# Optimization experiments

Measured on AMD Instinct MI355X. Metric: run time of the kernel, lower is better.

## Reference

```python
import jax, jax.numpy as jnp
import numpy as np

B, S = 8, 1024                      # num sequences, per-seq prefill length (uniform ragged batch)
NUM_HEADS, HEAD_DIM, NUM_KV_HEADS = 32, 128, 8
GROUP = NUM_HEADS // NUM_KV_HEADS   # GQA repeat factor
SCALE = 1.0 / float(np.sqrt(HEAD_DIM))
T = B * S                           # total tokens in batch
NUM_SLOTS = 16384                   # KV-cache slots
DKV = NUM_KV_HEADS * HEAD_DIM


def setup_inputs() -> dict:
    key = jax.random.key(0)
    ks = jax.random.split(key, 4)
    q = jax.random.normal(ks[0], (T, NUM_HEADS * HEAD_DIM), dtype=jnp.float32)
    k = jax.random.normal(ks[1], (T, DKV), dtype=jnp.float32)
    v = jax.random.normal(ks[2], (T, DKV), dtype=jnp.float32)
    k_cache = jnp.zeros((NUM_SLOTS, DKV), dtype=jnp.float32)
    v_cache = jnp.zeros((NUM_SLOTS, DKV), dtype=jnp.float32)
    # distinct slots per token (pure prefill: gather mapping == store mapping)
    slot_mapping = jax.random.permutation(ks[3], NUM_SLOTS)[:T].astype(jnp.int32)
    seq_slot_mapping = slot_mapping
    return {"q": q, "k": k, "v": v, "k_cache": k_cache, "v_cache": v_cache,
            "slot_mapping": slot_mapping, "seq_slot_mapping": seq_slot_mapping}


def reference(q, k, v, k_cache, v_cache, slot_mapping, seq_slot_mapping):
    # reshape to per-head layout
    kr = k.reshape(T, DKV)
    vr = v.reshape(T, DKV)
    # store_kvcache: scatter new k/v into paged cache by slot
    k_cache = k_cache.at[slot_mapping].set(kr)
    v_cache = v_cache.at[slot_mapping].set(vr)
    # get_kvcache: gather the per-sequence contiguous KV from the cache
    ck = k_cache[seq_slot_mapping].reshape(B, S, NUM_KV_HEADS, HEAD_DIM)
    cv = v_cache[seq_slot_mapping].reshape(B, S, NUM_KV_HEADS, HEAD_DIM)
    qb = q.reshape(B, S, NUM_HEADS, HEAD_DIM)
    # GQA: repeat_interleave kv heads (matches torch SDPA enable_gqa)
    ck = jnp.repeat(ck, GROUP, axis=2)  # [B,S,H,D]
    cv = jnp.repeat(cv, GROUP, axis=2)
    scores = jnp.einsum("bqhd,bkhd->bhqk", qb, ck) * SCALE  # [B,H,S,S]
    causal = jnp.tril(jnp.ones((S, S), dtype=bool))
    scores = jnp.where(causal[None, None], scores, jnp.finfo(scores.dtype).min)
    probs = jax.nn.softmax(scores, axis=-1)
    o = jnp.einsum("bhqk,bkhd->bqhd", probs, cv)  # [B,S,H,D]
    return o.reshape(T, NUM_HEADS * HEAD_DIM)
```

## Files before the change

kernel.cpp:

```cpp
#include <hip/hip_runtime.h>

#define NB 8
#define NS 1024
#define NH 32
#define NKV 8
#define ND 128
#define QT 256
#define KT 64

typedef _Float16 f16x8 __attribute__((ext_vector_type(8)));
typedef __fp16 fp16x2 __attribute__((ext_vector_type(2)));
typedef float f32x16 __attribute__((ext_vector_type(16)));
typedef unsigned int u32x2 __attribute__((ext_vector_type(2)));

__device__ __forceinline__ float exp2fast(float x) { return __builtin_amdgcn_exp2f(x); }
__device__ __forceinline__ unsigned pkrtz_u(float a, float b) {
  union { fp16x2 h; unsigned u; } c;
  c.h = __builtin_amdgcn_cvt_pkrtz(a, b);
  return c.u;
}
__device__ __forceinline__ u32x2 swap32(float x) {
  union { float f; unsigned u; } c; c.f = x;
  return __builtin_amdgcn_permlane32_swap(c.u, c.u, false, false);
}
__device__ __forceinline__ float asf(unsigned u) { union { unsigned u; float f; } c; c.u = u; return c.f; }

__global__ __launch_bounds__(256)
void cvt_kf(const float* __restrict__ kg, char* __restrict__ wsK)
{
  int g = blockIdx.x * 256 + threadIdx.x;
  int t = g >> 7, c8 = g & 127;
  int hkv = c8 >> 4, d8 = c8 & 15;
  const float* src = kg + (size_t)t * 1024 + hkv * 128 + d8 * 8;
  float4 a = *(const float4*)src;
  float4 c = *(const float4*)(src + 4);
  f16x8 h8;
  h8[0] = (_Float16)a.x; h8[1] = (_Float16)a.y; h8[2] = (_Float16)a.z; h8[3] = (_Float16)a.w;
  h8[4] = (_Float16)c.x; h8[5] = (_Float16)c.y; h8[6] = (_Float16)c.z; h8[7] = (_Float16)c.w;
  int b  = t >> 10, kv = t & 1023;
  int ti = kv >> 6, kvl = kv & 63, kb = kvl >> 5, lq = kvl & 31;
  int dblk = d8 >> 1, hi = d8 & 1;
  size_t off = (((size_t)(b * 8 + hkv) * 16 + ti) * 16 + kb * 8 + dblk) * 1024 + (hi * 32 + lq) * 16;
  *(f16x8*)(wsK + off) = h8;
}

__global__ __launch_bounds__(256)
void cvt_vf(const float* __restrict__ vg, _Float16* __restrict__ wsV)
{
  __shared__ _Float16 T[ND][KT];
  const int tid = threadIdx.x;
  const int kvt = blockIdx.x, b = blockIdx.y, hkv = blockIdx.z;
#pragma unroll
  for (int pass = 0; pass < 8; ++pass) {
    int kvr = (tid >> 5) + pass * 8;
    int d4  = (tid & 31) * 4;
    float4 v = ((const float4*)vg)[(size_t)(b * NS + kvt * KT + kvr) * 256 + hkv * 32 + (tid & 31)];
    T[d4 + 0][kvr] = (_Float16)v.x;
    T[d4 + 1][kvr] = (_Float16)v.y;
    T[d4 + 2][kvr] = (_Float16)v.z;
    T[d4 + 3][kvr] = (_Float16)v.w;
  }
  __syncthreads();
  _Float16* out = wsV + ((size_t)(b * 8 + hkv) * 16 + kvt) * 8192;
#pragma unroll
  for (int pass = 0; pass < 4; ++pass) {
    int unit = tid + pass * 256;
    int c = unit >> 6, lane = unit & 63;
    int d = (c & 3) * 32 + (lane & 31);
    int kv8 = (c >> 2) * 16 + (lane >> 5) * 8;
    *(f16x8*)(out + unit * 8) = *(const f16x8*)&T[d][kv8];
  }
}

__global__ __launch_bounds__(512, 1)
void attn_fwd(const float* __restrict__ qg, const char* __restrict__ wsK,
              const char* __restrict__ wsV, float* __restrict__ og)
{
  __shared__ __align__(16) char Klds[4][16384];
  __shared__ __align__(16) char Vlds[4][16384];

  const int id = blockIdx.x;
  const int v  = (id & 7) * 32 + (id >> 3);
  const int panel = v >> 2;
  const int sub   = v & 3;
  const int b     = panel >> 3;
  const int hkv   = panel & 7;
  const int h     = hkv * 4 + sub;

  const int tid  = threadIdx.x;
  const int lane = tid & 63;
  const int w    = tid >> 6;
  const int lq   = lane & 31;
  const int hi   = lane >> 5;

  const float QS = 0.08838834764831845f * 1.4426950408889634f;

  const char* wsKb = wsK + (size_t)panel * 16 * 16384;
  const char* wsVb = wsV + (size_t)panel * 16 * 16384;

  const int o0 = tid * 16;
  const int o1 = (tid + 512) * 16;

  f16x8 kpre0, kpre1, vpre0, vpre1;

  const int qorder[4] = {0, 3, 1, 2};

#pragma unroll 1
  for (int ph = 0; ph < 4; ++ph) {
    const int qtile = qorder[ph];
    const int wv    = (ph & 1) ? (7 - w) : w;
    const int qr0w  = qtile * QT + wv * 32;
    const int qrow  = qr0w + lq;

    f16x8 qf[8];
    {
      const float* qp = qg + (size_t)(b * NS + qrow) * (NH * ND) + h * ND + hi * 8;
#pragma unroll
      for (int dblk = 0; dblk < 8; ++dblk) {
        float4 f0 = *(const float4*)(qp + dblk * 16);
        float4 f1 = *(const float4*)(qp + dblk * 16 + 4);
        f16x8 a;
        a[0] = (_Float16)(f0.x * QS); a[1] = (_Float16)(f0.y * QS);
        a[2] = (_Float16)(f0.z * QS); a[3] = (_Float16)(f0.w * QS);
        a[4] = (_Float16)(f1.x * QS); a[5] = (_Float16)(f1.y * QS);
        a[6] = (_Float16)(f1.z * QS); a[7] = (_Float16)(f1.w * QS);
        qf[dblk] = a;
      }
    }

    f32x16 acc[4];
#pragma unroll
    for (int nb = 0; nb < 4; ++nb)
#pragma unroll
      for (int r = 0; r < 16; ++r) acc[nb][r] = 0.f;
    float m_run = -1e30f, l_run = 0.f;

    auto compute_tile = [&](int t) {
      const int kv0 = t * KT;
      if (kv0 > qr0w + 31) return;
      const char* Kb = &Klds[t & 3][0];
      const char* Vb = &Vlds[t & 3][0];

      f32x16 s[2];
#pragma unroll
      for (int r = 0; r < 16; ++r) { s[0][r] = 0.f; s[1][r] = 0.f; }
      __builtin_amdgcn_s_setprio(1);
#pragma unroll
      for (int dblk = 0; dblk < 8; ++dblk) {
        f16x8 k0 = *(const f16x8*)(Kb + dblk * 1024 + lane * 16);
        f16x8 k1 = *(const f16x8*)(Kb + (8 + dblk) * 1024 + lane * 16);
        s[0] = __builtin_amdgcn_mfma_f32_32x32x16_f16(k0, qf[dblk], s[0], 0, 0, 0);
        s[1] = __builtin_amdgcn_mfma_f32_32x32x16_f16(k1, qf[dblk], s[1], 0, 0, 0);
      }
      __builtin_amdgcn_s_setprio(0);

      if (kv0 + KT - 1 > qr0w) {
        const int thr = qrow - kv0;
#pragma unroll
        for (int kb = 0; kb < 2; ++kb)
#pragma unroll
          for (int r = 0; r < 16; ++r) {
            int kvl = kb * 32 + (r & 3) + 8 * (r >> 2) + 4 * hi;
            if (kvl > thr) s[kb][r] = -1e30f;
          }
      }

      float pmax = s[0][0];
#pragma unroll
      for (int r = 1; r < 16; ++r) pmax = fmaxf(pmax, s[0][r]);
#pragma unroll
      for (int r = 0; r < 16; ++r) pmax = fmaxf(pmax, s[1][r]);
      {
        u32x2 pr = swap32(pmax);
        pmax = fmaxf(asf(pr[0]), asf(pr[1]));
      }
      const int need = !__all(pmax <= m_run + 8.0f);
      if (need) {
        const float mn = fmaxf(m_run, pmax);
        const float al = exp2fast(m_run - mn);
        m_run = mn;
#pragma unroll
        for (int r = 0; r < 16; ++r) {
          int row = (r & 3) + 8 * (r >> 2) + 4 * hi;
          float a = __shfl(al, row, 64);
#pragma unroll
          for (int nb = 0; nb < 4; ++nb) acc[nb][r] *= a;
        }
        l_run *= al;
      }
      float rs = 0.f;
#pragma unroll
      for (int kb = 0; kb < 2; ++kb)
#pragma unroll
        for (int r = 0; r < 16; ++r) {
          float pv = exp2fast(s[kb][r] - m_run);
          s[kb][r] = pv;
          rs += pv;
        }
      {
        u32x2 sr = swap32(rs);
        rs = asf(sr[0]) + asf(sr[1]);
      }
      l_run += rs;

      f16x8 pa[4];
#pragma unroll
      for (int t4 = 0; t4 < 4; ++t4) {
        const int kb = t4 >> 1, rb = (t4 & 1) * 8;
        unsigned w0 = pkrtz_u(s[kb][rb + 0], s[kb][rb + 1]);
        unsigned w1 = pkrtz_u(s[kb][rb + 2], s[kb][rb + 3]);
        unsigned w2 = pkrtz_u(s[kb][rb + 4], s[kb][rb + 5]);
        unsigned w3 = pkrtz_u(s[kb][rb + 6], s[kb][rb + 7]);
        u32x2 p02 = __builtin_amdgcn_permlane32_swap(w0, w2, false, false);
        u32x2 p13 = __builtin_amdgcn_permlane32_swap(w1, w3, false, false);
        union { unsigned u[4]; f16x8 v; } pw;
        pw.u[0] = p02[0]; pw.u[1] = p13[0]; pw.u[2] = p02[1]; pw.u[3] = p13[1];
        pa[t4] = pw.v;
      }

      __builtin_amdgcn_s_setprio(1);
#pragma unroll
      for (int t4 = 0; t4 < 4; ++t4)
#pragma unroll
        for (int nb = 0; nb < 4; ++nb) {
          f16x8 vb = *(const f16x8*)(Vb + (t4 * 4 + nb) * 1024 + lane * 16);
          acc[nb] = __builtin_amdgcn_mfma_f32_32x32x16_f16(pa[t4], vb, acc[nb], 0, 0, 0);
        }
      __builtin_amdgcn_s_setprio(0);
    };

    const int npairs = 2 * (qtile + 1);

    kpre0 = *(const f16x8*)(wsKb + o0); kpre1 = *(const f16x8*)(wsKb + o1);
    vpre0 = *(const f16x8*)(wsVb + o0); vpre1 = *(const f16x8*)(wsVb + o1);
    *(f16x8*)(&Klds[0][0] + o0) = kpre0; *(f16x8*)(&Klds[0][0] + o1) = kpre1;
    *(f16x8*)(&Vlds[0][0] + o0) = vpre0; *(f16x8*)(&Vlds[0][0] + o1) = vpre1;
    kpre0 = *(const f16x8*)(wsKb + 16384 + o0); kpre1 = *(const f16x8*)(wsKb + 16384 + o1);
    vpre0 = *(const f16x8*)(wsVb + 16384 + o0); vpre1 = *(const f16x8*)(wsVb + 16384 + o1);
    *(f16x8*)(&Klds[1][0] + o0) = kpre0; *(f16x8*)(&Klds[1][0] + o1) = kpre1;
    *(f16x8*)(&Vlds[1][0] + o0) = vpre0; *(f16x8*)(&Vlds[1][0] + o1) = vpre1;
    asm volatile("s_waitcnt lgkmcnt(0)" ::: "memory");
    __builtin_amdgcn_s_barrier();
    __builtin_amdgcn_sched_barrier(0);

#pragma unroll 1
    for (int pj = 0; pj < npairs; ++pj) {
      const int a  = 2 * pj;
      const bool hn = (pj + 1 < npairs);
      const int t1 = (w & 1) ? a + 1 : a;
      const int t2 = (w & 1) ? a : a + 1;

      if (hn) {
        const char* gk = wsKb + (size_t)(a + 2) * 16384;
        const char* gv = wsVb + (size_t)(a + 2) * 16384;
        kpre0 = *(const f16x8*)(gk + o0); kpre1 = *(const f16x8*)(gk + o1);
        vpre0 = *(const f16x8*)(gv + o0); vpre1 = *(const f16x8*)(gv + o1);
      }

      compute_tile(t1);

      if (hn) {
        *(f16x8*)(&Klds[(a + 2) & 3][0] + o0) = kpre0;
        *(f16x8*)(&Klds[(a + 2) & 3][0] + o1) = kpre1;
        *(f16x8*)(&Vlds[(a + 2) & 3][0] + o0) = vpre0;
        *(f16x8*)(&Vlds[(a + 2) & 3][0] + o1) = vpre1;
        const char* gk = wsKb + (size_t)(a + 3) * 16384;
        const char* gv = wsVb + (size_t)(a + 3) * 16384;
        kpre0 = *(const f16x8*)(gk + o0); kpre1 = *(const f16x8*)(gk + o1);
        vpre0 = *(const f16x8*)(gv + o0); vpre1 = *(const f16x8*)(gv + o1);
      }

      compute_tile(t2);

      if (hn) {
        *(f16x8*)(&Klds[(a + 3) & 3][0] + o0) = kpre0;
        *(f16x8*)(&Klds[(a + 3) & 3][0] + o1) = kpre1;
        *(f16x8*)(&Vlds[(a + 3) & 3][0] + o0) = vpre0;
        *(f16x8*)(&Vlds[(a + 3) & 3][0] + o1) = vpre1;
      }

      asm volatile("s_waitcnt lgkmcnt(0)" ::: "memory");
      __builtin_amdgcn_s_barrier();
      __builtin_amdgcn_sched_barrier(0);
    }

    const float linv = 1.0f / l_run;
#pragma unroll
    for (int r = 0; r < 16; ++r) {
      int row = (r & 3) + 8 * (r >> 2) + 4 * hi;
      float li = __shfl(linv, row, 64);
      float* op = og + (size_t)(b * NS + qr0w + row) * (NH * ND) + h * ND + lq;
#pragma unroll
      for (int nb = 0; nb < 4; ++nb)
        op[nb * 32] = acc[nb][r] * li;
    }
    __builtin_amdgcn_s_barrier();
  }
}

extern "C" void kernel_launch(void* const* d_in, const int* in_sizes, int n_in,
                              void* d_out, int out_size, void* d_ws, size_t ws_size,
                              hipStream_t stream) {
  const float* q = (const float*)d_in[0];
  const float* k = (const float*)d_in[1];
  const float* v = (const float*)d_in[2];
  float* o = (float*)d_out;

  const size_t KSZ = (size_t)NB * NKV * NS * ND * sizeof(_Float16);
  if (ws_size < 2 * KSZ) return;
  char*     wsK = (char*)d_ws;
  _Float16* wsV = (_Float16*)((char*)d_ws + KSZ);

  cvt_kf<<<dim3((NB * NS * 128) / 256), 256, 0, stream>>>(k, wsK);
  cvt_vf<<<dim3(NS / KT, NB, NKV),      256, 0, stream>>>(v, wsV);
  attn_fwd<<<dim3(256),                 512, 0, stream>>>(q, wsK, (const char*)wsV, o);
}
```

Baseline: 157.7 us.

## Split tile compute into QK, softmax and PV stages and batch two tiles' QK

The per-tile compute lambda is split into separate QK-MFMA, softmax and PV-MFMA stages. Both tiles of a pair now run their QK products back to back, so the second tile's MFMAs can overlap the first tile's softmax. The per-wave alternating tile order is dropped. The prefetch for the second tile is now issued after both tiles finish rather than between them, which shortens the time available to hide global load latency and raises register pressure from keeping two score sets live.

```diff
diff --git a/kernel.cpp b/kernel.cpp
--- a/kernel.cpp
+++ b/kernel.cpp
@@ -135,41 +135,37 @@
       for (int r = 0; r < 16; ++r) acc[nb][r] = 0.f;
     float m_run = -1e30f, l_run = 0.f;
 
-    auto compute_tile = [&](int t) {
-      const int kv0 = t * KT;
-      if (kv0 > qr0w + 31) return;
+    auto qk_tile = [&](int t, f32x16& s0, f32x16& s1) {
       const char* Kb = &Klds[t & 3][0];
-      const char* Vb = &Vlds[t & 3][0];
-
-      f32x16 s[2];
-#pragma unroll
-      for (int r = 0; r < 16; ++r) { s[0][r] = 0.f; s[1][r] = 0.f; }
+#pragma unroll
+      for (int r = 0; r < 16; ++r) { s0[r] = 0.f; s1[r] = 0.f; }
       __builtin_amdgcn_s_setprio(1);
 #pragma unroll
       for (int dblk = 0; dblk < 8; ++dblk) {
         f16x8 k0 = *(const f16x8*)(Kb + dblk * 1024 + lane * 16);
         f16x8 k1 = *(const f16x8*)(Kb + (8 + dblk) * 1024 + lane * 16);
-        s[0] = __builtin_amdgcn_mfma_f32_32x32x16_f16(k0, qf[dblk], s[0], 0, 0, 0);
-        s[1] = __builtin_amdgcn_mfma_f32_32x32x16_f16(k1, qf[dblk], s[1], 0, 0, 0);
+        s0 = __builtin_amdgcn_mfma_f32_32x32x16_f16(k0, qf[dblk], s0, 0, 0, 0);
+        s1 = __builtin_amdgcn_mfma_f32_32x32x16_f16(k1, qf[dblk], s1, 0, 0, 0);
       }
       __builtin_amdgcn_s_setprio(0);
-
+    };
+
+    auto sm_tile = [&](int t, f32x16& s0, f32x16& s1, f16x8* pa) {
+      const int kv0 = t * KT;
       if (kv0 + KT - 1 > qr0w) {
         const int thr = qrow - kv0;
 #pragma unroll
-        for (int kb = 0; kb < 2; ++kb)
-#pragma unroll
-          for (int r = 0; r < 16; ++r) {
-            int kvl = kb * 32 + (r & 3) + 8 * (r >> 2) + 4 * hi;
-            if (kvl > thr) s[kb][r] = -1e30f;
-          }
-      }
-
-      float pmax = s[0][0];
-#pragma unroll
-      for (int r = 1; r < 16; ++r) pmax = fmaxf(pmax, s[0][r]);
-#pragma unroll
-      for (int r = 0; r < 16; ++r) pmax = fmaxf(pmax, s[1][r]);
+        for (int r = 0; r < 16; ++r) {
+          int kvl = (r & 3) + 8 * (r >> 2) + 4 * hi;
+          if (kvl > thr) s0[r] = -1e30f;
+          if (kvl + 32 > thr) s1[r] = -1e30f;
+        }
+      }
+      float pmax = s0[0];
+#pragma unroll
+      for (int r = 1; r < 16; ++r) pmax = fmaxf(pmax, s0[r]);
+#pragma unroll
+      for (int r = 0; r < 16; ++r) pmax = fmaxf(pmax, s1[r]);
       {
         u32x2 pr = swap32(pmax);
         pmax = fmaxf(asf(pr[0]), asf(pr[1]));
@@ -190,34 +186,38 @@
       }
       float rs = 0.f;
 #pragma unroll
-      for (int kb = 0; kb < 2; ++kb)
-#pragma unroll
-        for (int r = 0; r < 16; ++r) {
-          float pv = exp2fast(s[kb][r] - m_run);
-          s[kb][r] = pv;
-          rs += pv;
-        }
+      for (int r = 0; r < 16; ++r) {
+        float pv = exp2fast(s0[r] - m_run);
+        s0[r] = pv; rs += pv;
+      }
+#pragma unroll
+      for (int r = 0; r < 16; ++r) {
+        float pv = exp2fast(s1[r] - m_run);
+        s1[r] = pv; rs += pv;
+      }
       {
         u32x2 sr = swap32(rs);
         rs = asf(sr[0]) + asf(sr[1]);
       }
       l_run += rs;
-
-      f16x8 pa[4];
 #pragma unroll
       for (int t4 = 0; t4 < 4; ++t4) {
-        const int kb = t4 >> 1, rb = (t4 & 1) * 8;
-        unsigned w0 = pkrtz_u(s[kb][rb + 0], s[kb][rb + 1]);
-        unsigned w1 = pkrtz_u(s[kb][rb + 2], s[kb][rb + 3]);
-        unsigned w2 = pkrtz_u(s[kb][rb + 4], s[kb][rb + 5]);
-        unsigned w3 = pkrtz_u(s[kb][rb + 6], s[kb][rb + 7]);
+        const f32x16& sk = (t4 < 2) ? s0 : s1;
+        const int rb = (t4 & 1) * 8;
+        unsigned w0 = pkrtz_u(sk[rb + 0], sk[rb + 1]);
+        unsigned w1 = pkrtz_u(sk[rb + 2], sk[rb + 3]);
+        unsigned w2 = pkrtz_u(sk[rb + 4], sk[rb + 5]);
+        unsigned w3 = pkrtz_u(sk[rb + 6], sk[rb + 7]);
         u32x2 p02 = __builtin_amdgcn_permlane32_swap(w0, w2, false, false);
         u32x2 p13 = __builtin_amdgcn_permlane32_swap(w1, w3, false, false);
         union { unsigned u[4]; f16x8 v; } pw;
         pw.u[0] = p02[0]; pw.u[1] = p13[0]; pw.u[2] = p02[1]; pw.u[3] = p13[1];
         pa[t4] = pw.v;
       }
-
+    };
+
+    auto pv_tile = [&](int t, const f16x8* pa) {
+      const char* Vb = &Vlds[t & 3][0];
       __builtin_amdgcn_s_setprio(1);
 #pragma unroll
       for (int t4 = 0; t4 < 4; ++t4)
@@ -247,8 +247,8 @@
     for (int pj = 0; pj < npairs; ++pj) {
       const int a  = 2 * pj;
       const bool hn = (pj + 1 < npairs);
-      const int t1 = (w & 1) ? a + 1 : a;
-      const int t2 = (w & 1) ? a : a + 1;
+      const bool liveA = (a * KT <= qr0w + 31);
+      const bool liveB = ((a + 1) * KT <= qr0w + 31);
 
       if (hn) {
         const char* gk = wsKb + (size_t)(a + 2) * 16384;
@@ -257,7 +257,22 @@
         vpre0 = *(const f16x8*)(gv + o0); vpre1 = *(const f16x8*)(gv + o1);
       }
 
-      compute_tile(t1);
+      if (liveA) {
+        f32x16 sA0, sA1;
+        qk_tile(a, sA0, sA1);
+        f32x16 sB0, sB1;
+        if (liveB) qk_tile(a + 1, sB0, sB1);
+        {
+          f16x8 paA[4];
+          sm_tile(a, sA0, sA1, paA);
+          pv_tile(a, paA);
+        }
+        if (liveB) {
+          f16x8 paB[4];
+          sm_tile(a + 1, sB0, sB1, paB);
+          pv_tile(a + 1, paB);
+        }
+      }
 
       if (hn) {
         *(f16x8*)(&Klds[(a + 2) & 3][0] + o0) = kpre0;
@@ -268,11 +283,6 @@
         const char* gv = wsVb + (size_t)(a + 3) * 16384;
         kpre0 = *(const f16x8*)(gk + o0); kpre1 = *(const f16x8*)(gk + o1);
         vpre0 = *(const f16x8*)(gv + o0); vpre1 = *(const f16x8*)(gv + o1);
-      }
-
-      compute_tile(t2);
-
-      if (hn) {
         *(f16x8*)(&Klds[(a + 3) & 3][0] + o0) = kpre0;
         *(f16x8*)(&Klds[(a + 3) & 3][0] + o1) = kpre1;
         *(f16x8*)(&Vlds[(a + 3) & 3][0] + o0) = vpre0;
```

Result: slower. 170.4 us (+8.1%).
